# Kernel optimization log

Measured on AMD Instinct MI355X. Metric: run time of the kernel, lower is better.

The kernel has to match this reference:

```python
import jax, jax.numpy as jnp
import numpy as np
from jax import lax

BN_EPS = 1e-5
DIST_EPS = 1e-8

def _three_nn_interpolate(xyz1, xyz2, points2):
    # squared pairwise distances: (B, N, S)
    d2 = (jnp.sum(xyz1 ** 2, -1)[:, :, None]
          + jnp.sum(xyz2 ** 2, -1)[:, None, :]
          - 2.0 * jnp.einsum('bnd,bsd->bns', xyz1, xyz2))
    neg_d, idx = lax.top_k(-d2, 3)            # 3 nearest -> (B, N, 3)
    dist = -neg_d
    recip = 1.0 / (dist + DIST_EPS)
    weight = recip / jnp.sum(recip, -1, keepdims=True)   # (B, N, 3)
    gathered = jax.vmap(lambda p, i: p[i])(points2, idx)  # (B, N, 3, C2)
    return jnp.einsum('bnkc,bnk->bnc', gathered, weight)

def _conv_bn_relu(x, w, g, b):
    # x: (B, N, Cin); 1x1 conv == matmul; BatchNorm1d over (B, N) per channel (training stats)
    y = jnp.einsum('bnc,oc->bno', x, w)
    mu = jnp.mean(y, axis=(0, 1))
    var = jnp.mean((y - mu) ** 2, axis=(0, 1))
    yn = (y - mu) * lax.rsqrt(var + BN_EPS)
    return jax.nn.relu(yn * g + b)

def setup_inputs() -> dict:
    key = jax.random.key(0)
    ks = jax.random.split(key, 6)
    B, N, S, C1, C2 = 16, 4096, 1024, 256, 256
    return {
        'xyz1': jax.random.normal(ks[0], (B, N, 3), jnp.float32),
        'xyz2': jax.random.normal(ks[1], (B, S, 3), jnp.float32),
        'points1': jax.random.normal(ks[2], (B, N, C1), jnp.float32),
        'points2': jax.random.normal(ks[3], (B, S, C2), jnp.float32),
        'w1': jax.random.normal(ks[4], (256, C1 + C2), jnp.float32) * 0.04,
        'g1': jnp.ones((256,), jnp.float32),
        'b1': jnp.zeros((256,), jnp.float32),
        'w2': jax.random.normal(ks[5], (256, 256), jnp.float32) * 0.06,
        'g2': jnp.ones((256,), jnp.float32),
        'b2': jnp.zeros((256,), jnp.float32),
    }

def reference(xyz1, xyz2, points1, points2, w1, g1, b1, w2, g2, b2):
    interp = _three_nn_interpolate(xyz1, xyz2, points2)    # (B, N, C2)
    feats = jnp.concatenate([points1, interp], axis=-1)    # (B, N, C1+C2)
    h = _conv_bn_relu(feats, w1, g1, b1)
    out = _conv_bn_relu(h, w2, g2, b2)
    return out                                              # (B, N, 256)
```

## Files before the change

### kernel.cpp

```cpp
#include <hip/hip_runtime.h>
#include <stdint.h>

typedef unsigned short ushort_t;
typedef __bf16 bf16x8 __attribute__((ext_vector_type(8)));
typedef float f32x4 __attribute__((ext_vector_type(4)));
typedef unsigned short ushort8 __attribute__((ext_vector_type(8)));

#define DEV static __device__ __forceinline__

DEV unsigned short f2bf(float f) {
    union { float f; unsigned int i; } v; v.f = f;
    unsigned int u = v.i;
    return (unsigned short)((u + 0x7fffu + ((u >> 16) & 1u)) >> 16);
}
DEV float bf2f(unsigned short u) {
    union { unsigned int i; float f; } v; v.i = ((unsigned int)u) << 16; return v.f;
}

__global__ __launch_bounds__(256) void cvt_kernel(
    const float* __restrict__ in, ushort_t* __restrict__ out, int n)
{
    int i = blockIdx.x * 256 + threadIdx.x;
    if (i < n) out[i] = f2bf(in[i]);
}

__global__ __launch_bounds__(256) void knn_kernel(
    const float* __restrict__ xyz1, const float* __restrict__ xyz2,
    int* __restrict__ idx_out, float* __restrict__ w_out)
{
    __shared__ float4 P[1024];
    __shared__ float mD[12][64];
    __shared__ int   mI[12][64];
    const int b = blockIdx.y;
    const int tid = threadIdx.x;
    for (int s = tid; s < 1024; s += 256) {
        const float* p = xyz2 + ((size_t)b * 1024 + s) * 3;
        float x = p[0], y = p[1], z = p[2];
        float pp = __fadd_rn(__fadd_rn(__fmul_rn(x, x), __fmul_rn(y, y)), __fmul_rn(z, z));
        P[s] = make_float4(x, y, z, pp);
    }
    __syncthreads();
    const int ql = tid & 63;
    const int chunk = tid >> 6;
    const int n = blockIdx.x * 64 + ql;
    const float* q = xyz1 + ((size_t)b * 4096 + n) * 3;
    float qx = q[0], qy = q[1], qz = q[2];
    float qq = __fadd_rn(__fadd_rn(__fmul_rn(qx, qx), __fmul_rn(qy, qy)), __fmul_rn(qz, qz));
    float d0 = 1e30f, d1 = 1e30f, d2 = 1e30f;
    int i0 = 0, i1 = 0, i2 = 0;
    const int s0 = chunk * 256;
#pragma unroll 4
    for (int s = s0; s < s0 + 256; ++s) {
        float4 p = P[s];
        float dot = __fadd_rn(__fadd_rn(__fmul_rn(qx, p.x), __fmul_rn(qy, p.y)), __fmul_rn(qz, p.z));
        float d = __fsub_rn(__fadd_rn(qq, p.w), __fmul_rn(2.0f, dot));
        if (d < d2) {
            if (d < d1) {
                d2 = d1; i2 = i1;
                if (d < d0) { d1 = d0; i1 = i0; d0 = d; i0 = s; }
                else        { d1 = d;  i1 = s; }
            } else { d2 = d; i2 = s; }
        }
    }
    mD[chunk * 3 + 0][ql] = d0; mI[chunk * 3 + 0][ql] = i0;
    mD[chunk * 3 + 1][ql] = d1; mI[chunk * 3 + 1][ql] = i1;
    mD[chunk * 3 + 2][ql] = d2; mI[chunk * 3 + 2][ql] = i2;
    __syncthreads();
    if (tid < 64) {
        float e0 = 1e30f, e1 = 1e30f, e2 = 1e30f;
        int j0 = 0, j1 = 0, j2 = 0;
#pragma unroll
        for (int c = 0; c < 12; ++c) {
            float d = mD[c][ql]; int i = mI[c][ql];
            if (d < e2) {
                if (d < e1) {
                    e2 = e1; j2 = j1;
                    if (d < e0) { e1 = e0; j1 = j0; e0 = d; j0 = i; }
                    else        { e1 = d;  j1 = i; }
                } else { e2 = d; j2 = i; }
            }
        }
        float r0 = 1.0f / (e0 + 1e-8f);
        float r1 = 1.0f / (e1 + 1e-8f);
        float r2 = 1.0f / (e2 + 1e-8f);
        float rs = __fadd_rn(__fadd_rn(r0, r1), r2);
        size_t o = ((size_t)b * 4096 + n) * 3;
        idx_out[o + 0] = j0; idx_out[o + 1] = j1; idx_out[o + 2] = j2;
        w_out[o + 0] = r0 / rs; w_out[o + 1] = r1 / rs; w_out[o + 2] = r2 / rs;
    }
}

DEV void cvt8(const float4& u0, const float4& u1, ushort8& hv) {
    hv[0] = f2bf(u0.x); hv[1] = f2bf(u0.y); hv[2] = f2bf(u0.z); hv[3] = f2bf(u0.w);
    hv[4] = f2bf(u1.x); hv[5] = f2bf(u1.y); hv[6] = f2bf(u1.z); hv[7] = f2bf(u1.w);
}

__global__ __launch_bounds__(256) void gemm1_kernel(
    const float* __restrict__ p1, const float* __restrict__ points2,
    const int* __restrict__ idx, const float* __restrict__ wgt,
    const ushort_t* __restrict__ w1b, ushort_t* __restrict__ y,
    float* __restrict__ sums, float* __restrict__ sqs)
{
    __shared__ ushort_t As[64 * 512];
    const int tid = threadIdx.x;
    const int wave = tid >> 6, lane = tid & 63;
    const int frl = lane & 15, fq = lane >> 4;
    const int fr7 = frl & 7;
    const int m0 = blockIdx.x * 64;

    {
        const int r = tid >> 2, cg = tid & 3;
        ushort_t* dst = As + r * 512;
        const float4* gp = (const float4*)(p1 + (size_t)(m0 + r) * 256 + cg * 64);
#pragma unroll
        for (int jj = 0; jj < 8; ++jj) {
            float4 u0 = gp[2 * jj], u1 = gp[2 * jj + 1];
            ushort8 hv; cvt8(u0, u1, hv);
            int cb = cg * 8 + jj;
            *(ushort8*)(dst + ((cb ^ (r & 7)) << 3)) = hv;
        }
        const size_t qo = (size_t)(m0 + r) * 3;
        int i0 = idx[qo], i1 = idx[qo + 1], i2 = idx[qo + 2];
        float w0 = wgt[qo], w1 = wgt[qo + 1], w2 = wgt[qo + 2];
        const float* pb = points2 + (size_t)(m0 >> 12) * (1024 * 256);
        const float4* g0 = (const float4*)(pb + (size_t)i0 * 256 + cg * 64);
        const float4* g1 = (const float4*)(pb + (size_t)i1 * 256 + cg * 64);
        const float4* g2 = (const float4*)(pb + (size_t)i2 * 256 + cg * 64);
#pragma unroll
        for (int jj = 0; jj < 8; ++jj) {
            float4 a0 = g0[2 * jj], a1 = g0[2 * jj + 1];
            float4 b0 = g1[2 * jj], b1 = g1[2 * jj + 1];
            float4 c0 = g2[2 * jj], c1 = g2[2 * jj + 1];
            float v[8];
            v[0] = fmaf(w2, c0.x, fmaf(w1, b0.x, __fmul_rn(w0, a0.x)));
            v[1] = fmaf(w2, c0.y, fmaf(w1, b0.y, __fmul_rn(w0, a0.y)));
            v[2] = fmaf(w2, c0.z, fmaf(w1, b0.z, __fmul_rn(w0, a0.z)));
            v[3] = fmaf(w2, c0.w, fmaf(w1, b0.w, __fmul_rn(w0, a0.w)));
            v[4] = fmaf(w2, c1.x, fmaf(w1, b1.x, __fmul_rn(w0, a1.x)));
            v[5] = fmaf(w2, c1.y, fmaf(w1, b1.y, __fmul_rn(w0, a1.y)));
            v[6] = fmaf(w2, c1.z, fmaf(w1, b1.z, __fmul_rn(w0, a1.z)));
            v[7] = fmaf(w2, c1.w, fmaf(w1, b1.w, __fmul_rn(w0, a1.w)));
            ushort8 hv;
#pragma unroll
            for (int j = 0; j < 8; ++j) hv[j] = f2bf(v[j]);
            int cb = 32 + cg * 8 + jj;
            *(ushort8*)(dst + ((cb ^ (r & 7)) << 3)) = hv;
        }
    }

    f32x4 acc[4][4];
#pragma unroll
    for (int i = 0; i < 4; ++i)
#pragma unroll
        for (int j = 0; j < 4; ++j) acc[i][j] = f32x4{0.0f, 0.0f, 0.0f, 0.0f};

    __syncthreads();

    const ushort_t* wb = w1b + (size_t)(wave * 64 + frl) * 512 + fq * 8;
    bf16x8 aA[4], aB[4], bA[4], bB[4];

#define LOADB1(dst, kc) { _Pragma("unroll") \
    for (int j = 0; j < 4; ++j) dst[j] = *(const bf16x8*)(wb + j * (16 * 512) + (kc) * 32); }
#define LOADA1(dst, kc) { _Pragma("unroll") \
    for (int i = 0; i < 4; ++i) dst[i] = *(const bf16x8*)(As + (i * 16 + frl) * 512 + (((((kc) << 2) + fq) ^ fr7) << 3)); }
#define MF16(a, b) { _Pragma("unroll") \
    for (int i = 0; i < 4; ++i) { _Pragma("unroll") \
        for (int j = 0; j < 4; ++j) \
            acc[i][j] = __builtin_amdgcn_mfma_f32_16x16x32_bf16(a[i], b[j], acc[i][j], 0, 0, 0); } }

    LOADA1(aA, 0); LOADB1(bA, 0);
#pragma unroll
    for (int kc = 0; kc < 16; kc += 2) {
        LOADA1(aB, kc + 1); LOADB1(bB, kc + 1);
        MF16(aA, bA);
        if (kc + 2 < 16) { LOADA1(aA, kc + 2); LOADB1(bA, kc + 2); }
        MF16(aB, bB);
    }

#pragma unroll
    for (int j = 0; j < 4; ++j) {
        const int col = wave * 64 + j * 16 + frl;
        float s = 0.f, q = 0.f;
#pragma unroll
        for (int i = 0; i < 4; ++i)
#pragma unroll
            for (int rr = 0; rr < 4; ++rr) {
                ushort_t hb = f2bf(acc[i][j][rr]);
                float v = bf2f(hb);
                y[(size_t)(m0 + i * 16 + fq * 4 + rr) * 256 + col] = hb;
                s += v; q = fmaf(v, v, q);
            }
        s += __shfl_xor(s, 16); s += __shfl_xor(s, 32);
        q += __shfl_xor(q, 16); q += __shfl_xor(q, 32);
        if (fq == 0) { atomicAdd(&sums[col], s); atomicAdd(&sqs[col], q); }
    }
}

__global__ __launch_bounds__(256) void gemm2_kernel(
    const ushort_t* __restrict__ y1, const ushort_t* __restrict__ w2b,
    const float* __restrict__ a1, const float* __restrict__ c1,
    float* __restrict__ y2, float* __restrict__ sums, float* __restrict__ sqs)
{
    __shared__ ushort_t As[64 * 264];
    __shared__ float sA[256], sC[256];
    const int tid = threadIdx.x;
    const int wave = tid >> 6, lane = tid & 63;
    const int frl = lane & 15, fq = lane >> 4;
    const int m0 = blockIdx.x * 64;

    sA[tid] = a1[tid]; sC[tid] = c1[tid];
    __syncthreads();

    {
        const int r = tid >> 2, cg = tid & 3;
        const ushort8* gp = (const ushort8*)(y1 + (size_t)(m0 + r) * 256 + cg * 64);
        ushort_t* dst = As + r * 264 + cg * 64;
#pragma unroll
        for (int jj = 0; jj < 8; ++jj) {
            ushort8 raw = gp[jj];
            ushort8 hv;
#pragma unroll
            for (int j = 0; j < 8; ++j) {
                int ch = cg * 64 + jj * 8 + j;
                float v = bf2f(raw[j]);
                hv[j] = f2bf(fmaxf(fmaf(v, sA[ch], sC[ch]), 0.0f));
            }
            *(ushort8*)(dst + jj * 8) = hv;
        }
    }

    f32x4 acc[4][4];
#pragma unroll
    for (int i = 0; i < 4; ++i)
#pragma unroll
        for (int j = 0; j < 4; ++j) acc[i][j] = f32x4{0.0f, 0.0f, 0.0f, 0.0f};

    __syncthreads();

    const ushort_t* wb = w2b + (size_t)(wave * 64 + frl) * 256 + fq * 8;
    bf16x8 aA[4], aB[4], bA[4], bB[4];

#define LOADB2(dst, kc) { _Pragma("unroll") \
    for (int j = 0; j < 4; ++j) dst[j] = *(const bf16x8*)(wb + j * (16 * 256) + (kc) * 32); }
#define LOADA2(dst, kc) { _Pragma("unroll") \
    for (int i = 0; i < 4; ++i) dst[i] = *(const bf16x8*)(As + (i * 16 + frl) * 264 + (kc) * 32 + fq * 8); }

    LOADA2(aA, 0); LOADB2(bA, 0);
#pragma unroll
    for (int kc = 0; kc < 8; kc += 2) {
        LOADA2(aB, kc + 1); LOADB2(bB, kc + 1);
        MF16(aA, bA);
        if (kc + 2 < 8) { LOADA2(aA, kc + 2); LOADB2(bA, kc + 2); }
        MF16(aB, bB);
    }

#pragma unroll
    for (int j = 0; j < 4; ++j) {
        const int col = wave * 64 + j * 16 + frl;
        float s = 0.f, q = 0.f;
#pragma unroll
        for (int i = 0; i < 4; ++i)
#pragma unroll
            for (int rr = 0; rr < 4; ++rr) {
                float v = acc[i][j][rr];
                y2[(size_t)(m0 + i * 16 + fq * 4 + rr) * 256 + col] = v;
                s += v; q = fmaf(v, v, q);
            }
        s += __shfl_xor(s, 16); s += __shfl_xor(s, 32);
        q += __shfl_xor(q, 16); q += __shfl_xor(q, 32);
        if (fq == 0) { atomicAdd(&sums[col], s); atomicAdd(&sqs[col], q); }
    }
}

__global__ __launch_bounds__(256) void finalize_kernel(
    const float* __restrict__ sums, const float* __restrict__ sqs,
    const float* __restrict__ g, const float* __restrict__ bias,
    float* __restrict__ a, float* __restrict__ c)
{
    const int ch = threadIdx.x;
    const float inv_n = 1.0f / 65536.0f;
    float mu = sums[ch] * inv_n;
    float var = fmaf(-mu, mu, sqs[ch] * inv_n);
    float is = 1.0f / sqrtf(var + 1e-5f);
    float aa = g[ch] * is;
    a[ch] = aa;
    c[ch] = fmaf(-mu, aa, bias[ch]);
}

__global__ __launch_bounds__(256) void apply_kernel(
    float* __restrict__ y2, const float* __restrict__ a, const float* __restrict__ c)
{
    const size_t i = ((size_t)blockIdx.x * 256 + threadIdx.x) * 4;
    const int ch = (int)(i & 255);
    float4 v = *(const float4*)(y2 + i);
    const float4 av = *(const float4*)(a + ch);
    const float4 cv = *(const float4*)(c + ch);
    v.x = fmaxf(fmaf(v.x, av.x, cv.x), 0.0f);
    v.y = fmaxf(fmaf(v.y, av.y, cv.y), 0.0f);
    v.z = fmaxf(fmaf(v.z, av.z, cv.z), 0.0f);
    v.w = fmaxf(fmaf(v.w, av.w, cv.w), 0.0f);
    *(float4*)(y2 + i) = v;
}

extern "C" void kernel_launch(void* const* d_in, const int* in_sizes, int n_in,
                              void* d_out, int out_size, void* d_ws, size_t ws_size,
                              hipStream_t stream)
{
    const float* xyz1    = (const float*)d_in[0];
    const float* xyz2    = (const float*)d_in[1];
    const float* points1 = (const float*)d_in[2];
    const float* points2 = (const float*)d_in[3];
    const float* w1      = (const float*)d_in[4];
    const float* g1      = (const float*)d_in[5];
    const float* b1      = (const float*)d_in[6];
    const float* w2      = (const float*)d_in[7];
    const float* g2      = (const float*)d_in[8];
    const float* b2      = (const float*)d_in[9];
    float* out = (float*)d_out;

    char* ws = (char*)d_ws;
    float* sums1 = (float*)(ws + 0);
    float* sqs1  = (float*)(ws + 1024);
    float* a1    = (float*)(ws + 2048);
    float* c1    = (float*)(ws + 3072);
    float* sums2 = (float*)(ws + 4096);
    float* sqs2  = (float*)(ws + 5120);
    float* a2    = (float*)(ws + 6144);
    float* c2    = (float*)(ws + 7168);
    ushort_t* w1b = (ushort_t*)(ws + (64u << 10));
    ushort_t* w2b = (ushort_t*)(ws + (320u << 10));
    int*   idx   = (int*)(ws + (1u << 20));
    float* wgt   = (float*)(ws + (2u << 20));
    ushort_t* y1 = (ushort_t*)(ws + (4u << 20));

    hipMemsetAsync(ws, 0, 8192, stream);
    cvt_kernel<<<dim3(512), 256, 0, stream>>>(w1, w1b, 131072);
    cvt_kernel<<<dim3(256), 256, 0, stream>>>(w2, w2b, 65536);
    knn_kernel<<<dim3(64, 16), 256, 0, stream>>>(xyz1, xyz2, idx, wgt);
    gemm1_kernel<<<dim3(1024), 256, 0, stream>>>(points1, points2, idx, wgt, w1b, y1, sums1, sqs1);
    finalize_kernel<<<dim3(1), 256, 0, stream>>>(sums1, sqs1, g1, b1, a1, c1);
    gemm2_kernel<<<dim3(1024), 256, 0, stream>>>(y1, w2b, a1, c1, out, sums2, sqs2);
    finalize_kernel<<<dim3(1), 256, 0, stream>>>(sums2, sqs2, g2, b2, a2, c2);
    apply_kernel<<<dim3(16384), 256, 0, stream>>>(out, a2, c2);
}
```

Measured before the change: 309.7 us.

## Split interpolation into its own kernel and restructure GEMMs with LDS-staged K tiles

Converts points2 to bf16 up front and adds a separate interpolation kernel that writes a bf16 interpolated feature buffer, so gemm1 no longer gathers fp32 neighbours itself. Both GEMMs change from 64-row tiles holding the full K in LDS to 32-row tiles that loop over K in 32-wide chunks, staging weight tiles into LDS with global_load_lds. The KNN kernel is reshaped to 32 queries per block with 8 chunks. The aim is smaller LDS use and higher occupancy, but it adds extra kernel launches, an intermediate buffer round trip, and two barriers per K-step with no double buffering. Rounding points2 to bf16 before the weighted sum also slightly changes the numerics.

```diff
diff --git a/kernel.cpp b/kernel.cpp
--- a/kernel.cpp
+++ b/kernel.cpp
@@ -5,6 +5,9 @@
 typedef __bf16 bf16x8 __attribute__((ext_vector_type(8)));
 typedef float f32x4 __attribute__((ext_vector_type(4)));
 typedef unsigned short ushort8 __attribute__((ext_vector_type(8)));
+typedef unsigned short ushort4_t __attribute__((ext_vector_type(4)));
+typedef __attribute__((address_space(1))) void GVoid;
+typedef __attribute__((address_space(3))) void LVoid;
 
 #define DEV static __device__ __forceinline__
 
@@ -24,13 +27,23 @@
     if (i < n) out[i] = f2bf(in[i]);
 }
 
+__global__ __launch_bounds__(256) void cvt4_kernel(
+    const float* __restrict__ in, ushort_t* __restrict__ out)
+{
+    int i = (blockIdx.x * 256 + threadIdx.x) * 4;
+    float4 v = *(const float4*)(in + i);
+    ushort4_t o;
+    o[0] = f2bf(v.x); o[1] = f2bf(v.y); o[2] = f2bf(v.z); o[3] = f2bf(v.w);
+    *(ushort4_t*)(out + i) = o;
+}
+
 __global__ __launch_bounds__(256) void knn_kernel(
     const float* __restrict__ xyz1, const float* __restrict__ xyz2,
     int* __restrict__ idx_out, float* __restrict__ w_out)
 {
     __shared__ float4 P[1024];
-    __shared__ float mD[12][64];
-    __shared__ int   mI[12][64];
+    __shared__ float mD[24][32];
+    __shared__ int   mI[24][32];
     const int b = blockIdx.y;
     const int tid = threadIdx.x;
     for (int s = tid; s < 1024; s += 256) {
@@ -40,17 +53,17 @@
         P[s] = make_float4(x, y, z, pp);
     }
     __syncthreads();
-    const int ql = tid & 63;
-    const int chunk = tid >> 6;
-    const int n = blockIdx.x * 64 + ql;
+    const int ql = tid & 31;
+    const int chunk = tid >> 5;
+    const int n = blockIdx.x * 32 + ql;
     const float* q = xyz1 + ((size_t)b * 4096 + n) * 3;
     float qx = q[0], qy = q[1], qz = q[2];
     float qq = __fadd_rn(__fadd_rn(__fmul_rn(qx, qx), __fmul_rn(qy, qy)), __fmul_rn(qz, qz));
     float d0 = 1e30f, d1 = 1e30f, d2 = 1e30f;
     int i0 = 0, i1 = 0, i2 = 0;
-    const int s0 = chunk * 256;
+    const int s0 = chunk * 128;
 #pragma unroll 4
-    for (int s = s0; s < s0 + 256; ++s) {
+    for (int s = s0; s < s0 + 128; ++s) {
         float4 p = P[s];
         float dot = __fadd_rn(__fadd_rn(__fmul_rn(qx, p.x), __fmul_rn(qy, p.y)), __fmul_rn(qz, p.z));
         float d = __fsub_rn(__fadd_rn(qq, p.w), __fmul_rn(2.0f, dot));
@@ -66,11 +79,11 @@
     mD[chunk * 3 + 1][ql] = d1; mI[chunk * 3 + 1][ql] = i1;
     mD[chunk * 3 + 2][ql] = d2; mI[chunk * 3 + 2][ql] = i2;
     __syncthreads();
-    if (tid < 64) {
+    if (tid < 32) {
         float e0 = 1e30f, e1 = 1e30f, e2 = 1e30f;
         int j0 = 0, j1 = 0, j2 = 0;
 #pragma unroll
-        for (int c = 0; c < 12; ++c) {
+        for (int c = 0; c < 24; ++c) {
             float d = mD[c][ql]; int i = mI[c][ql];
             if (d < e2) {
                 if (d < e1) {
@@ -90,91 +103,91 @@
     }
 }
 
+__global__ __launch_bounds__(256) void interp_kernel(
+    const ushort_t* __restrict__ p2b, const int* __restrict__ idx,
+    const float* __restrict__ wgt, ushort_t* __restrict__ itp)
+{
+    const int t = blockIdx.x * 256 + threadIdx.x;
+    const int q = t >> 3;
+    const int cg = (t & 7) * 32;
+    const size_t o = (size_t)q * 3;
+    int i0 = idx[o], i1 = idx[o + 1], i2 = idx[o + 2];
+    float w0 = wgt[o], w1 = wgt[o + 1], w2 = wgt[o + 2];
+    const ushort_t* pb = p2b + (size_t)(q >> 12) * (1024 * 256);
+    const ushort8* g0 = (const ushort8*)(pb + (size_t)i0 * 256 + cg);
+    const ushort8* g1 = (const ushort8*)(pb + (size_t)i1 * 256 + cg);
+    const ushort8* g2 = (const ushort8*)(pb + (size_t)i2 * 256 + cg);
+    ushort8* dst = (ushort8*)(itp + (size_t)q * 256 + cg);
+#pragma unroll
+    for (int s = 0; s < 4; ++s) {
+        ushort8 a = g0[s], b = g1[s], c = g2[s];
+        ushort8 ov;
+#pragma unroll
+        for (int j = 0; j < 8; ++j) {
+            float acc = __fmul_rn(w0, bf2f(a[j]));
+            acc = fmaf(w1, bf2f(b[j]), acc);
+            acc = fmaf(w2, bf2f(c[j]), acc);
+            ov[j] = f2bf(acc);
+        }
+        dst[s] = ov;
+    }
+}
+
 DEV void cvt8(const float4& u0, const float4& u1, ushort8& hv) {
     hv[0] = f2bf(u0.x); hv[1] = f2bf(u0.y); hv[2] = f2bf(u0.z); hv[3] = f2bf(u0.w);
     hv[4] = f2bf(u1.x); hv[5] = f2bf(u1.y); hv[6] = f2bf(u1.z); hv[7] = f2bf(u1.w);
 }
 
 __global__ __launch_bounds__(256) void gemm1_kernel(
-    const float* __restrict__ p1, const float* __restrict__ points2,
-    const int* __restrict__ idx, const float* __restrict__ wgt,
+    const float* __restrict__ p1, const ushort_t* __restrict__ itp,
     const ushort_t* __restrict__ w1b, ushort_t* __restrict__ y,
     float* __restrict__ sums, float* __restrict__ sqs)
 {
-    __shared__ ushort_t As[64 * 512];
+    __shared__ __align__(16) ushort_t As[32 * 40];
+    __shared__ __align__(16) ushort_t Bs[256 * 32];
     const int tid = threadIdx.x;
     const int wave = tid >> 6, lane = tid & 63;
     const int frl = lane & 15, fq = lane >> 4;
-    const int fr7 = frl & 7;
-    const int m0 = blockIdx.x * 64;
-
-    {
-        const int r = tid >> 2, cg = tid & 3;
-        ushort_t* dst = As + r * 512;
-        const float4* gp = (const float4*)(p1 + (size_t)(m0 + r) * 256 + cg * 64);
-#pragma unroll
-        for (int jj = 0; jj < 8; ++jj) {
-            float4 u0 = gp[2 * jj], u1 = gp[2 * jj + 1];
-            ushort8 hv; cvt8(u0, u1, hv);
-            int cb = cg * 8 + jj;
-            *(ushort8*)(dst + ((cb ^ (r & 7)) << 3)) = hv;
-        }
-        const size_t qo = (size_t)(m0 + r) * 3;
-        int i0 = idx[qo], i1 = idx[qo + 1], i2 = idx[qo + 2];
-        float w0 = wgt[qo], w1 = wgt[qo + 1], w2 = wgt[qo + 2];
-        const float* pb = points2 + (size_t)(m0 >> 12) * (1024 * 256);
-        const float4* g0 = (const float4*)(pb + (size_t)i0 * 256 + cg * 64);
-        const float4* g1 = (const float4*)(pb + (size_t)i1 * 256 + cg * 64);
-        const float4* g2 = (const float4*)(pb + (size_t)i2 * 256 + cg * 64);
-#pragma unroll
-        for (int jj = 0; jj < 8; ++jj) {
-            float4 a0 = g0[2 * jj], a1 = g0[2 * jj + 1];
-            float4 b0 = g1[2 * jj], b1 = g1[2 * jj + 1];
-            float4 c0 = g2[2 * jj], c1 = g2[2 * jj + 1];
-            float v[8];
-            v[0] = fmaf(w2, c0.x, fmaf(w1, b0.x, __fmul_rn(w0, a0.x)));
-            v[1] = fmaf(w2, c0.y, fmaf(w1, b0.y, __fmul_rn(w0, a0.y)));
-            v[2] = fmaf(w2, c0.z, fmaf(w1, b0.z, __fmul_rn(w0, a0.z)));
-            v[3] = fmaf(w2, c0.w, fmaf(w1, b0.w, __fmul_rn(w0, a0.w)));
-            v[4] = fmaf(w2, c1.x, fmaf(w1, b1.x, __fmul_rn(w0, a1.x)));
-            v[5] = fmaf(w2, c1.y, fmaf(w1, b1.y, __fmul_rn(w0, a1.y)));
-            v[6] = fmaf(w2, c1.z, fmaf(w1, b1.z, __fmul_rn(w0, a1.z)));
-            v[7] = fmaf(w2, c1.w, fmaf(w1, b1.w, __fmul_rn(w0, a1.w)));
+    const int m0 = blockIdx.x * 32;
+    const int sr = tid >> 2, sq = tid & 3;
+
+    f32x4 acc[2][4];
+#pragma unroll
+    for (int i = 0; i < 2; ++i)
+#pragma unroll
+        for (int j = 0; j < 4; ++j) acc[i][j] = f32x4{0.0f, 0.0f, 0.0f, 0.0f};
+
+    for (int kc = 0; kc < 16; ++kc) {
+        __syncthreads();
+#pragma unroll
+        for (int p = 0; p < 4; ++p) {
+            const ushort_t* g = w1b + (size_t)(p * 64 + sr) * 512 + kc * 32 + sq * 8;
+            __builtin_amdgcn_global_load_lds((GVoid*)g, (LVoid*)(Bs + p * 2048 + wave * 512), 16, 0, 0);
+        }
+        if (tid < 128) {
             ushort8 hv;
-#pragma unroll
-            for (int j = 0; j < 8; ++j) hv[j] = f2bf(v[j]);
-            int cb = 32 + cg * 8 + jj;
-            *(ushort8*)(dst + ((cb ^ (r & 7)) << 3)) = hv;
-        }
-    }
-
-    f32x4 acc[4][4];
-#pragma unroll
-    for (int i = 0; i < 4; ++i)
-#pragma unroll
-        for (int j = 0; j < 4; ++j) acc[i][j] = f32x4{0.0f, 0.0f, 0.0f, 0.0f};
-
-    __syncthreads();
-
-    const ushort_t* wb = w1b + (size_t)(wave * 64 + frl) * 512 + fq * 8;
-    bf16x8 aA[4], aB[4], bA[4], bB[4];
-
-#define LOADB1(dst, kc) { _Pragma("unroll") \
-    for (int j = 0; j < 4; ++j) dst[j] = *(const bf16x8*)(wb + j * (16 * 512) + (kc) * 32); }
-#define LOADA1(dst, kc) { _Pragma("unroll") \
-    for (int i = 0; i < 4; ++i) dst[i] = *(const bf16x8*)(As + (i * 16 + frl) * 512 + (((((kc) << 2) + fq) ^ fr7) << 3)); }
-#define MF16(a, b) { _Pragma("unroll") \
-    for (int i = 0; i < 4; ++i) { _Pragma("unroll") \
-        for (int j = 0; j < 4; ++j) \
-            acc[i][j] = __builtin_amdgcn_mfma_f32_16x16x32_bf16(a[i], b[j], acc[i][j], 0, 0, 0); } }
-
-    LOADA1(aA, 0); LOADB1(bA, 0);
-#pragma unroll
-    for (int kc = 0; kc < 16; kc += 2) {
-        LOADA1(aB, kc + 1); LOADB1(bB, kc + 1);
-        MF16(aA, bA);
-        if (kc + 2 < 16) { LOADA1(aA, kc + 2); LOADB1(bA, kc + 2); }
-        MF16(aB, bB);
+            if (kc < 8) {
+                const float4* g = (const float4*)(p1 + (size_t)(m0 + sr) * 256 + kc * 32 + sq * 8);
+                float4 u0 = g[0], u1 = g[1];
+                cvt8(u0, u1, hv);
+            } else {
+                hv = *(const ushort8*)(itp + (size_t)(m0 + sr) * 256 + (kc - 8) * 32 + sq * 8);
+            }
+            *(ushort8*)(As + sr * 40 + sq * 8) = hv;
+        }
+        __syncthreads();
+        bf16x8 af[2], bfr[4];
+#pragma unroll
+        for (int i = 0; i < 2; ++i)
+            af[i] = *(const bf16x8*)(As + (i * 16 + frl) * 40 + fq * 8);
+#pragma unroll
+        for (int j = 0; j < 4; ++j)
+            bfr[j] = *(const bf16x8*)(Bs + (wave * 64 + j * 16 + frl) * 32 + fq * 8);
+#pragma unroll
+        for (int i = 0; i < 2; ++i)
+#pragma unroll
+            for (int j = 0; j < 4; ++j)
+                acc[i][j] = __builtin_amdgcn_mfma_f32_16x16x32_bf16(af[i], bfr[j], acc[i][j], 0, 0, 0);
     }
 
 #pragma unroll
@@ -182,7 +195,7 @@
         const int col = wave * 64 + j * 16 + frl;
         float s = 0.f, q = 0.f;
 #pragma unroll
-        for (int i = 0; i < 4; ++i)
+        for (int i = 0; i < 2; ++i)
 #pragma unroll
             for (int rr = 0; rr < 4; ++rr) {
                 ushort_t hb = f2bf(acc[i][j][rr]);
@@ -201,57 +214,54 @@
     const float* __restrict__ a1, const float* __restrict__ c1,
     float* __restrict__ y2, float* __restrict__ sums, float* __restrict__ sqs)
 {
-    __shared__ ushort_t As[64 * 264];
+    __shared__ __align__(16) ushort_t As[32 * 40];
+    __shared__ __align__(16) ushort_t Bs[256 * 32];
     __shared__ float sA[256], sC[256];
     const int tid = threadIdx.x;
     const int wave = tid >> 6, lane = tid & 63;
     const int frl = lane & 15, fq = lane >> 4;
-    const int m0 = blockIdx.x * 64;
+    const int m0 = blockIdx.x * 32;
+    const int sr = tid >> 2, sq = tid & 3;
 
     sA[tid] = a1[tid]; sC[tid] = c1[tid];
-    __syncthreads();
-
-    {
-        const int r = tid >> 2, cg = tid & 3;
-        const ushort8* gp = (const ushort8*)(y1 + (size_t)(m0 + r) * 256 + cg * 64);
-        ushort_t* dst = As + r * 264 + cg * 64;
-#pragma unroll
-        for (int jj = 0; jj < 8; ++jj) {
-            ushort8 raw = gp[jj];
+
+    f32x4 acc[2][4];
+#pragma unroll
+    for (int i = 0; i < 2; ++i)
+#pragma unroll
+        for (int j = 0; j < 4; ++j) acc[i][j] = f32x4{0.0f, 0.0f, 0.0f, 0.0f};
+
+    for (int kc = 0; kc < 8; ++kc) {
+        __syncthreads();
+#pragma unroll
+        for (int p = 0; p < 4; ++p) {
+            const ushort_t* g = w2b + (size_t)(p * 64 + sr) * 256 + kc * 32 + sq * 8;
+            __builtin_amdgcn_global_load_lds((GVoid*)g, (LVoid*)(Bs + p * 2048 + wave * 512), 16, 0, 0);
+        }
+        if (tid < 128) {
+            ushort8 raw = *(const ushort8*)(y1 + (size_t)(m0 + sr) * 256 + kc * 32 + sq * 8);
+            const int ch = kc * 32 + sq * 8;
             ushort8 hv;
 #pragma unroll
             for (int j = 0; j < 8; ++j) {
-                int ch = cg * 64 + jj * 8 + j;
                 float v = bf2f(raw[j]);
-                hv[j] = f2bf(fmaxf(fmaf(v, sA[ch], sC[ch]), 0.0f));
-            }
-            *(ushort8*)(dst + jj * 8) = hv;
-        }
-    }
-
-    f32x4 acc[4][4];
-#pragma unroll
-    for (int i = 0; i < 4; ++i)
-#pragma unroll
-        for (int j = 0; j < 4; ++j) acc[i][j] = f32x4{0.0f, 0.0f, 0.0f, 0.0f};
-
-    __syncthreads();
-
-    const ushort_t* wb = w2b + (size_t)(wave * 64 + frl) * 256 + fq * 8;
-    bf16x8 aA[4], aB[4], bA[4], bB[4];
-
-#define LOADB2(dst, kc) { _Pragma("unroll") \
-    for (int j = 0; j < 4; ++j) dst[j] = *(const bf16x8*)(wb + j * (16 * 256) + (kc) * 32); }
-#define LOADA2(dst, kc) { _Pragma("unroll") \
-    for (int i = 0; i < 4; ++i) dst[i] = *(const bf16x8*)(As + (i * 16 + frl) * 264 + (kc) * 32 + fq * 8); }
-
-    LOADA2(aA, 0); LOADB2(bA, 0);
-#pragma unroll
-    for (int kc = 0; kc < 8; kc += 2) {
-        LOADA2(aB, kc + 1); LOADB2(bB, kc + 1);
-        MF16(aA, bA);
-        if (kc + 2 < 8) { LOADA2(aA, kc + 2); LOADB2(bA, kc + 2); }
-        MF16(aB, bB);
+                hv[j] = f2bf(fmaxf(fmaf(v, sA[ch + j], sC[ch + j]), 0.0f));
+            }
+            *(ushort8*)(As + sr * 40 + sq * 8) = hv;
+        }
+        __syncthreads();
+        bf16x8 af[2], bfr[4];
+#pragma unroll
+        for (int i = 0; i < 2; ++i)
+            af[i] = *(const bf16x8*)(As + (i * 16 + frl) * 40 + fq * 8);
+#pragma unroll
+        for (int j = 0; j < 4; ++j)
+            bfr[j] = *(const bf16x8*)(Bs + (wave * 64 + j * 16 + frl) * 32 + fq * 8);
+#pragma unroll
+        for (int i = 0; i < 2; ++i)
+#pragma unroll
+            for (int j = 0; j < 4; ++j)
+                acc[i][j] = __builtin_amdgcn_mfma_f32_16x16x32_bf16(af[i], bfr[j], acc[i][j], 0, 0, 0);
     }
 
 #pragma unroll
@@ -259,7 +269,7 @@
         const int col = wave * 64 + j * 16 + frl;
         float s = 0.f, q = 0.f;
 #pragma unroll
-        for (int i = 0; i < 4; ++i)
+        for (int i = 0; i < 2; ++i)
 #pragma unroll
             for (int rr = 0; rr < 4; ++rr) {
                 float v = acc[i][j][rr];
@@ -329,17 +339,21 @@
     float* c2    = (float*)(ws + 7168);
     ushort_t* w1b = (ushort_t*)(ws + (64u << 10));
     ushort_t* w2b = (ushort_t*)(ws + (320u << 10));
-    int*   idx   = (int*)(ws + (1u << 20));
-    float* wgt   = (float*)(ws + (2u << 20));
-    ushort_t* y1 = (ushort_t*)(ws + (4u << 20));
+    ushort_t* p2b = (ushort_t*)(ws + (1u << 20));
+    int*   idx   = (int*)(ws + (10u << 20));
+    float* wgt   = (float*)(ws + (11u << 20));
+    ushort_t* itp = (ushort_t*)(ws + (12u << 20));
+    ushort_t* y1  = (ushort_t*)(ws + (44u << 20));
 
     hipMemsetAsync(ws, 0, 8192, stream);
     cvt_kernel<<<dim3(512), 256, 0, stream>>>(w1, w1b, 131072);
     cvt_kernel<<<dim3(256), 256, 0, stream>>>(w2, w2b, 65536);
-    knn_kernel<<<dim3(64, 16), 256, 0, stream>>>(xyz1, xyz2, idx, wgt);
-    gemm1_kernel<<<dim3(1024), 256, 0, stream>>>(points1, points2, idx, wgt, w1b, y1, sums1, sqs1);
+    cvt4_kernel<<<dim3(4096), 256, 0, stream>>>(points2, p2b);
+    knn_kernel<<<dim3(128, 16), 256, 0, stream>>>(xyz1, xyz2, idx, wgt);
+    interp_kernel<<<dim3(2048), 256, 0, stream>>>(p2b, idx, wgt, itp);
+    gemm1_kernel<<<dim3(2048), 256, 0, stream>>>(points1, itp, w1b, y1, sums1, sqs1);
     finalize_kernel<<<dim3(1), 256, 0, stream>>>(sums1, sqs1, g1, b1, a1, c1);
-    gemm2_kernel<<<dim3(1024), 256, 0, stream>>>(y1, w2b, a1, c1, out, sums2, sqs2);
+    gemm2_kernel<<<dim3(2048), 256, 0, stream>>>(y1, w2b, a1, c1, out, sums2, sqs2);
     finalize_kernel<<<dim3(1), 256, 0, stream>>>(sums2, sqs2, g2, b2, a2, c2);
     apply_kernel<<<dim3(16384), 256, 0, stream>>>(out, a2, c2);
 }
```

Result: slower. 360.9 us (+16.6%).
